# Kernel optimization log

Measured on AMD Instinct MI355X. Metric: run time of the kernel, lower is better.

The kernel has to match this reference:

```python
import math
import jax, jax.numpy as jnp
import numpy as np

N_HEAD = 32
LAYER_NUMBER = 10  # cancels out: beta*alibi*L + alpha*QK^T*L = alibi + QK^T/sqrt(d)


def build_alibi(seq_len, n_head, dtype):
    # Faithful port of BLOOM's build_alibi_tensor -> [n_head, 1, seq_len]
    cp2 = 2 ** math.floor(math.log2(n_head))
    base = 2.0 ** (-(2.0 ** -(math.log2(cp2) - 3)))
    slopes = base ** np.arange(1, 1 + cp2)
    if cp2 != n_head:
        extra_base = 2.0 ** (-(2.0 ** -(math.log2(2 * cp2) - 3)))
        num_rem = min(cp2, n_head - cp2)
        slopes = np.concatenate([slopes, extra_base ** np.arange(1, 1 + 2 * num_rem, 2)])
    alibi = slopes[:, None, None] * np.arange(seq_len)[None, None, :]
    return jnp.asarray(alibi, dtype)


def setup_inputs() -> dict:
    key = jax.random.key(0)
    ks = jax.random.split(key, 6)
    B, S, H = 4, 1024, 4096
    return {
        "hidden_states": jax.random.normal(ks[0], (B, S, H), jnp.float32),
        "residual": jax.random.normal(ks[1], (B, S, H), jnp.float32),
        "qkv_w": jax.random.normal(ks[2], (3 * H, H), jnp.float32) * 0.02,
        "qkv_b": jnp.zeros((3 * H,), jnp.float32),
        "dense_w": jax.random.normal(ks[3], (H, H), jnp.float32) * 0.02,
        "dense_b": jnp.zeros((H,), jnp.float32),
    }


def reference(hidden_states, residual, qkv_w, qkv_b, dense_w, dense_b):
    B, S, H = hidden_states.shape
    nh = N_HEAD
    d = H // nh
    # fused qkv projection: [B,S,3H] -> [B,S,nh,3d] -> split
    mixed = (hidden_states @ qkv_w.T + qkv_b).reshape(B, S, nh, 3 * d)
    q, k, v = jnp.split(mixed, 3, axis=-1)  # each [B,S,nh,d]

    alibi = build_alibi(S, nh, hidden_states.dtype)  # [nh,1,S]
    # beta*alibi + alpha*QK^T, then *layer_number in scaled softmax == alibi + QK^T/sqrt(d)
    scores = jnp.einsum("bqhd,bkhd->bhqk", q, k) / math.sqrt(d) + alibi[None]  # [B,nh,S,S]

    causal = jnp.tril(jnp.ones((S, S), bool))  # [S,S], True = attend
    scores = jnp.where(causal, scores, jnp.asarray(-10000.0, scores.dtype))
    # softmax in fp32 (attention_softmax_in_fp32), then zero masked entries like *(~padded_causal_mask)
    probs = jax.nn.softmax(scores.astype(jnp.float32), axis=-1) * causal
    probs = probs.astype(v.dtype)

    ctx = jnp.einsum("bhqk,bkhd->bqhd", probs, v).reshape(B, S, H)
    out = ctx @ dense_w.T + dense_b + residual  # dropout_add with p=0 / eval
    return out
```

## Files before the change

### kernel.cpp

```cpp
#include <hip/hip_runtime.h>
#include <hip/hip_bf16.h>

typedef __attribute__((ext_vector_type(8))) short bf16x8;
typedef __attribute__((ext_vector_type(4))) short short4v;
typedef __attribute__((ext_vector_type(4))) float f32x4;

#define MFMA16(A, B, C) __builtin_amdgcn_mfma_f32_16x16x32_bf16((A), (B), (C), 0, 0, 0)
#define GLDS16(g, l)                                                            \
  __builtin_amdgcn_global_load_lds(                                             \
      (const __attribute__((address_space(1))) void*)(g),                       \
      (__attribute__((address_space(3))) void*)(l), 16, 0, 0)

__device__ __forceinline__ short f2bf(float f) {
  union { float f; unsigned u; } v; v.f = f;
  return (short)((v.u + 0x7fffu + ((v.u >> 16) & 1u)) >> 16);
}

__device__ __forceinline__ void blk_barrier() {
  asm volatile("" ::: "memory");
  __builtin_amdgcn_s_barrier();
  asm volatile("" ::: "memory");
}

__global__ __launch_bounds__(256) void cvt_kernel(const float* __restrict__ in,
                                                  short* __restrict__ out, int n4) {
  int i = blockIdx.x * 256 + threadIdx.x;
  const int stride = gridDim.x * 256;
  for (; i < n4; i += stride) {
    f32x4 v = ((const f32x4*)in)[i];
    short4v o;
    o[0] = f2bf(v[0]); o[1] = f2bf(v[1]); o[2] = f2bf(v[2]); o[3] = f2bf(v[3]);
    ((short4v*)out)[i] = o;
  }
}

__global__ __launch_bounds__(512, 2) void gemm_bt8(const short* __restrict__ A,
                                                   const short* __restrict__ B,
                                                   const float* __restrict__ bias,
                                                   const float* __restrict__ resid,
                                                   short* __restrict__ Cb,
                                                   float* __restrict__ Cf,
                                                   int Mtiles, int Nn, int K, int mode) {
  __shared__ short sA[2][2][8192];
  __shared__ short sB[2][2][8192];
  const int tid = threadIdx.x;
  const int w = tid >> 6, l = tid & 63;
  const int wm = w >> 2, wn = w & 3;
  const int fr = l & 15, g4 = l >> 4, sx = l & 7;

  const int nwg = gridDim.x;
  const int qq = nwg >> 3, rr = nwg & 7;
  const int xcd = blockIdx.x & 7, sub = blockIdx.x >> 3;
  const int swz = (xcd < rr ? xcd * (qq + 1) : rr * (qq + 1) + (xcd - rr) * qq) + sub;
  const int rowBase = (swz % Mtiles) * 256;
  const int colBase = (swz / Mtiles) * 256;

  const int NT = K >> 6;
  const int swcol = ((l & 7) ^ (l >> 3)) * 8;
  const short* Ag = A + (size_t)(rowBase + w * 8 + (l >> 3)) * K + swcol;
  const short* Bg = B + (size_t)(colBase + w * 8 + (l >> 3)) * K + swcol;
  const size_t q1 = (size_t)64 * K;
  const size_t hh = (size_t)128 * K;

#define STAGE_A(buf, h, ko)                                     \
  GLDS16(Ag + (h) * hh + (ko), &sA[buf][h][w * 512]);           \
  GLDS16(Ag + (h) * hh + q1 + (ko), &sA[buf][h][(8 + w) * 512]);
#define STAGE_B(buf, h, ko)                                     \
  GLDS16(Bg + (h) * hh + (ko), &sB[buf][h][w * 512]);           \
  GLDS16(Bg + (h) * hh + q1 + (ko), &sB[buf][h][(8 + w) * 512]);
#define RD_A(buf, m, ks) \
  (*(const bf16x8*)&sA[buf][wm][(((m) * 16 + fr) << 6) + ((((ks) * 4 + g4) ^ sx) << 3)])
#define RD_B(buf, nf, ks) \
  (*(const bf16x8*)&sB[buf][wn >> 1][((((wn & 1) * 64) + (nf) * 16 + fr) << 6) + ((((ks) * 4 + g4) ^ sx) << 3)])

  f32x4 acc[8][4];
#pragma unroll
  for (int m = 0; m < 8; m++)
#pragma unroll
    for (int n = 0; n < 4; n++) acc[m][n] = (f32x4)(0.0f);

  STAGE_A(0, 0, 0); STAGE_A(0, 1, 0);
  STAGE_B(0, 0, 0); STAGE_B(0, 1, 0);

  for (int t = 0; t < NT; ++t) {
    const int cur = t & 1, nxt = cur ^ 1;
    const size_t ko = (size_t)(t + 1) << 6;
    bf16x8 bfr[4][2], af[2][2];
    if (t + 1 < NT) {
      STAGE_A(nxt, 0, ko); STAGE_A(nxt, 1, ko);
      asm volatile("s_waitcnt vmcnt(4)" ::: "memory");
    } else {
      asm volatile("s_waitcnt vmcnt(0)" ::: "memory");
    }
    blk_barrier();
#pragma unroll
    for (int nf = 0; nf < 4; nf++) {
      bfr[nf][0] = RD_B(cur, nf, 0);
      bfr[nf][1] = RD_B(cur, nf, 1);
    }
    af[0][0] = RD_A(cur, 0, 0); af[0][1] = RD_A(cur, 0, 1);
    af[1][0] = RD_A(cur, 1, 0); af[1][1] = RD_A(cur, 1, 1);
    __builtin_amdgcn_s_setprio(1);
#pragma unroll
    for (int mi = 0; mi < 2; mi++)
#pragma unroll
      for (int nf = 0; nf < 4; nf++) {
        acc[mi][nf] = MFMA16(af[mi][0], bfr[nf][0], acc[mi][nf]);
        acc[mi][nf] = MFMA16(af[mi][1], bfr[nf][1], acc[mi][nf]);
      }
    __builtin_amdgcn_s_setprio(0);
    blk_barrier();
#pragma unroll
    for (int p = 1; p < 4; p++) {
      af[0][0] = RD_A(cur, 2 * p, 0);     af[0][1] = RD_A(cur, 2 * p, 1);
      af[1][0] = RD_A(cur, 2 * p + 1, 0); af[1][1] = RD_A(cur, 2 * p + 1, 1);
      if (p == 1 && t + 1 < NT) {
        STAGE_B(nxt, 0, ko); STAGE_B(nxt, 1, ko);
      }
      blk_barrier();
      __builtin_amdgcn_s_setprio(1);
#pragma unroll
      for (int mi = 0; mi < 2; mi++)
#pragma unroll
        for (int nf = 0; nf < 4; nf++) {
          acc[2 * p + mi][nf] = MFMA16(af[mi][0], bfr[nf][0], acc[2 * p + mi][nf]);
          acc[2 * p + mi][nf] = MFMA16(af[mi][1], bfr[nf][1], acc[2 * p + mi][nf]);
        }
      __builtin_amdgcn_s_setprio(0);
      blk_barrier();
    }
  }

#pragma unroll
  for (int m = 0; m < 8; m++) {
    const int row0 = rowBase + wm * 128 + m * 16 + g4 * 4;
#pragma unroll
    for (int n = 0; n < 4; n++) {
      const int col = colBase + wn * 64 + n * 16 + fr;
      const float bc = bias[col];
#pragma unroll
      for (int j = 0; j < 4; j++) {
        const size_t idx = (size_t)(row0 + j) * Nn + col;
        const float v = acc[m][n][j] + bc;
        if (mode == 0) Cb[idx] = f2bf(v);
        else Cf[idx] = v + resid[idx];
      }
    }
  }
#undef STAGE_A
#undef STAGE_B
#undef RD_A
#undef RD_B
}

__global__ __launch_bounds__(512, 4) void gemm_bt(const short* __restrict__ A,
                                                  const short* __restrict__ B,
                                                  const float* __restrict__ bias,
                                                  const float* __restrict__ resid,
                                                  short* __restrict__ Cb,
                                                  float* __restrict__ Cf,
                                                  int Mtiles, int Nn, int K, int mode) {
  __shared__ short sA[2][128 * 32];
  __shared__ short sB[2][256 * 32];
  const int tid = threadIdx.x;
  const int w = tid >> 6, l = tid & 63;
  const int wm = w >> 2, wn = w & 3;
  const int fr = l & 15, g4 = l >> 4;
  const int slotx = (g4 ^ ((fr >> 1) & 3)) << 3;

  const int nwg = gridDim.x;
  const int qq = nwg >> 3, rr = nwg & 7;
  const int xcd = blockIdx.x & 7, sub = blockIdx.x >> 3;
  const int swz = (xcd < rr ? xcd * (qq + 1) : rr * (qq + 1) + (xcd - rr) * qq) + sub;
  const int rowBase = (swz % Mtiles) * 128;
  const int colBase = (swz / Mtiles) * 256;

  const int NT = K >> 5;
  const int scol = ((l & 3) ^ ((l >> 3) & 3)) << 3;
  const short* Ag = A + (size_t)(rowBase + w * 16 + (l >> 2)) * K + scol;
  const short* Bg0 = B + (size_t)(colBase + w * 16 + (l >> 2)) * K + scol;
  const short* Bg1 = Bg0 + (size_t)128 * K;

  f32x4 acc[4][4];
#pragma unroll
  for (int m = 0; m < 4; m++)
#pragma unroll
    for (int n = 0; n < 4; n++) acc[m][n] = (f32x4)(0.0f);

  GLDS16(Ag, &sA[0][w * 512]);
  GLDS16(Bg0, &sB[0][w * 512]);
  GLDS16(Bg1, &sB[0][(8 + w) * 512]);

  for (int t = 0; t < NT; ++t) {
    const int cur = t & 1, nxt = cur ^ 1;
    const int ko = (t + 1) << 5;
    if (t + 1 < NT) {
      GLDS16(Ag + ko, &sA[nxt][w * 512]);
      GLDS16(Bg0 + ko, &sB[nxt][w * 512]);
      GLDS16(Bg1 + ko, &sB[nxt][(8 + w) * 512]);
      asm volatile("s_waitcnt vmcnt(3)" ::: "memory");
    } else {
      asm volatile("s_waitcnt vmcnt(0)" ::: "memory");
    }
    blk_barrier();

    bf16x8 af[4], bfr[4];
#pragma unroll
    for (int m = 0; m < 4; m++)
      af[m] = *(const bf16x8*)&sA[cur][(wm * 64 + m * 16 + fr) * 32 + slotx];
#pragma unroll
    for (int nf = 0; nf < 4; nf++)
      bfr[nf] = *(const bf16x8*)&sB[cur][(wn * 64 + nf * 16 + fr) * 32 + slotx];
    __builtin_amdgcn_s_setprio(1);
#pragma unroll
    for (int m = 0; m < 4; m++)
#pragma unroll
      for (int nf = 0; nf < 4; nf++)
        acc[m][nf] = MFMA16(af[m], bfr[nf], acc[m][nf]);
    __builtin_amdgcn_s_setprio(0);
    blk_barrier();
  }

#pragma unroll
  for (int m = 0; m < 4; m++) {
    const int row0 = rowBase + wm * 64 + m * 16 + g4 * 4;
#pragma unroll
    for (int n = 0; n < 4; n++) {
      const int col = colBase + wn * 64 + n * 16 + fr;
      const float bc = bias[col];
#pragma unroll
      for (int j = 0; j < 4; j++) {
        const size_t idx = (size_t)(row0 + j) * Nn + col;
        const float v = acc[m][n][j] + bc;
        if (mode == 0) Cb[idx] = f2bf(v);
        else Cf[idx] = v + resid[idx];
      }
    }
  }
}

__global__ __launch_bounds__(256) void vtrans_kernel(const short* __restrict__ mixed,
                                                     short* __restrict__ vt) {
  __shared__ short tl[64][132];
  const int tid = threadIdx.x;
  const int st = blockIdx.x;
  const int bh = blockIdx.y;
  const int b = bh >> 5, h = bh & 31;
  const short* src = mixed + (size_t)(b * 1024 + st * 64) * 12288 + h * 384 + 256;
#pragma unroll
  for (int it = 0; it < 8; it++) {
    int idx = (tid + it * 256) * 4;
    int row = idx >> 7, col = idx & 127;
    *(short4v*)&tl[row][col] = *(const short4v*)(src + row * 12288 + col);
  }
  __syncthreads();
  short* dst = vt + (size_t)bh * 128 * 1024 + st * 64;
#pragma unroll
  for (int it = 0; it < 8; it++) {
    int o = (tid + it * 256) * 4;
    int d = o >> 6, t4 = o & 63;
    short4v w;
    w[0] = tl[t4][d]; w[1] = tl[t4 + 1][d]; w[2] = tl[t4 + 2][d]; w[3] = tl[t4 + 3][d];
    *(short4v*)(dst + d * 1024 + t4) = w;
  }
}

__global__ __launch_bounds__(256, 2) void attn_kernel(const short* __restrict__ mixed,
                                                      const short* __restrict__ vt,
                                                      short* __restrict__ ctx) {
  __shared__ short sK[2][64 * 128];
  __shared__ short sV[2][128 * 64];
  __shared__ unsigned p_lds[4][16 * 36];
  const int tid = threadIdx.x;
  const int w = tid >> 6, l = tid & 63;
  const int g = l >> 4, f = l & 15, f7 = l & 7;

  const int bidx = blockIdx.x;
  const int xcd = bidx & 7, idx = bidx >> 3;
  const int bh = (xcd << 4) | (idx >> 4);
  const int qt = idx & 15;
  const int b = bh >> 5, h = bh & 31;
  const int qw = qt * 64 + w * 16;
  const float scale = 0.08838834764831845f;
  const float slope = exp2f(-0.25f * (float)(h + 1));

  const short* qptr = mixed + (size_t)b * 1024 * 12288 + h * 384;
  const short* kptr = qptr + 128;
  const short* vtp = vt + (size_t)bh * 128 * 1024;

  bf16x8 qf[4];
  {
    const short* qrow = qptr + (size_t)(qw + f) * 12288 + (g << 3);
#pragma unroll
    for (int ks = 0; ks < 4; ks++) qf[ks] = *(const bf16x8*)(qrow + ks * 32);
  }

#define STAGE_K(buf, kt)                                                        \
  {                                                                             \
    _Pragma("unroll") for (int c4 = 0; c4 < 4; c4++) {                          \
      const int c = c4 * 4 + w;                                                 \
      const int r = c * 4 + (l >> 4);                                           \
      GLDS16(kptr + (size_t)((kt) + r) * 12288 + (((l & 15) ^ (r & 7)) << 3),   \
             &sK[buf][c << 9]);                                                 \
    }                                                                           \
  }
#define STAGE_V(buf, kt)                                                        \
  {                                                                             \
    _Pragma("unroll") for (int c4 = 0; c4 < 4; c4++) {                          \
      const int c = c4 * 4 + w;                                                 \
      const int r = c * 8 + (l >> 3);                                           \
      GLDS16(vtp + (size_t)r * 1024 + (kt) + (((l & 7) ^ (r & 7)) << 3),        \
             &sV[buf][c << 9]);                                                 \
    }                                                                           \
  }

  f32x4 acc[8];
#pragma unroll
  for (int n = 0; n < 8; n++) acc[n] = (f32x4)(0.0f);
  float mrun = -1e30f, lrun = 0.0f;
  const int q = qw + f;
  unsigned* pw = p_lds[w];

  const int TT = qt + 1;
  STAGE_K(0, 0);
  STAGE_V(0, 0);

  for (int t = 0; t < TT; ++t) {
    const int cur = t & 1, nxt = cur ^ 1;
    const int kt = t << 6;
    if (t + 1 < TT) {
      STAGE_K(nxt, kt + 64);
      STAGE_V(nxt, kt + 64);
      asm volatile("s_waitcnt vmcnt(8)" ::: "memory");
    } else {
      asm volatile("s_waitcnt vmcnt(0)" ::: "memory");
    }
    blk_barrier();

    f32x4 s[4];
#pragma unroll
    for (int ksub = 0; ksub < 4; ksub++) {
      s[ksub] = (f32x4)(0.0f);
      const int r = ksub * 16 + f;
#pragma unroll
      for (int ks = 0; ks < 4; ks++) {
        bf16x8 kf = *(const bf16x8*)&sK[cur][(r << 7) + ((((ks << 2) + g) ^ f7) << 3)];
        s[ksub] = MFMA16(kf, qf[ks], s[ksub]);
      }
    }

    float ev[4][4];
    float tmax = -1e30f;
#pragma unroll
    for (int ksub = 0; ksub < 4; ksub++)
#pragma unroll
      for (int j = 0; j < 4; j++) {
        const int k = kt + ksub * 16 + g * 4 + j;
        float v = s[ksub][j] * scale + slope * (float)k;
        if (k > q) v = -1e30f;
        ev[ksub][j] = v;
        tmax = fmaxf(tmax, v);
      }
    tmax = fmaxf(tmax, __shfl_xor(tmax, 16));
    tmax = fmaxf(tmax, __shfl_xor(tmax, 32));
    const float mnew = fmaxf(mrun, tmax);
    const float asc = __expf(mrun - mnew);
    float psum = 0.0f;
    unsigned* pr = pw + f * 36;
#pragma unroll
    for (int ksub = 0; ksub < 4; ksub++) {
      float e0 = __expf(ev[ksub][0] - mnew);
      float e1 = __expf(ev[ksub][1] - mnew);
      float e2 = __expf(ev[ksub][2] - mnew);
      float e3 = __expf(ev[ksub][3] - mnew);
      psum += (e0 + e1) + (e2 + e3);
      unsigned w0 = (unsigned)(unsigned short)f2bf(e0) |
                    ((unsigned)(unsigned short)f2bf(e1) << 16);
      unsigned w1 = (unsigned)(unsigned short)f2bf(e2) |
                    ((unsigned)(unsigned short)f2bf(e3) << 16);
      pr[ksub * 8 + g * 2] = w0;
      pr[ksub * 8 + g * 2 + 1] = w1;
    }
    psum += __shfl_xor(psum, 16);
    psum += __shfl_xor(psum, 32);
    lrun = lrun * asc + psum;
    mrun = mnew;

    float ascB[4];
#pragma unroll
    for (int j = 0; j < 4; j++) ascB[j] = __shfl(asc, 20 * g + j);
#pragma unroll
    for (int n = 0; n < 8; n++)
#pragma unroll
      for (int j = 0; j < 4; j++) acc[n][j] *= ascB[j];

    bf16x8 pa0 = *(const bf16x8*)(pw + f * 36 + (g << 2));
    bf16x8 pa1 = *(const bf16x8*)(pw + f * 36 + 16 + (g << 2));
#pragma unroll
    for (int n = 0; n < 8; n++) {
      const int dr = (n << 4) + f;
      bf16x8 vf0 = *(const bf16x8*)&sV[cur][(dr << 6) + ((g ^ f7) << 3)];
      acc[n] = MFMA16(pa0, vf0, acc[n]);
      bf16x8 vf1 = *(const bf16x8*)&sV[cur][(dr << 6) + (((4 + g) ^ f7) << 3)];
      acc[n] = MFMA16(pa1, vf1, acc[n]);
    }
    blk_barrier();
  }

  const float linv = 1.0f / lrun;
  float invB[4];
#pragma unroll
  for (int j = 0; j < 4; j++) invB[j] = __shfl(linv, 20 * g + j);
  const int trow = b * 1024 + qw + (g << 2);
#pragma unroll
  for (int n = 0; n < 8; n++) {
    const int col = h * 128 + (n << 4) + f;
#pragma unroll
    for (int j = 0; j < 4; j++)
      ctx[(size_t)(trow + j) * 4096 + col] = f2bf(acc[n][j] * invB[j]);
  }
#undef STAGE_K
#undef STAGE_V
}

extern "C" void kernel_launch(void* const* d_in, const int* in_sizes, int n_in,
                              void* d_out, int out_size, void* d_ws, size_t ws_size,
                              hipStream_t stream) {
  const float* hs = (const float*)d_in[0];
  const float* resid = (const float*)d_in[1];
  const float* qkv_w = (const float*)d_in[2];
  const float* qkv_b = (const float*)d_in[3];
  const float* dense_w = (const float*)d_in[4];
  const float* dense_b = (const float*)d_in[5];
  float* out = (float*)d_out;

  short* hs_b = (short*)d_ws;
  short* wqkv_b = hs_b + (size_t)16777216;
  short* wd_b = wqkv_b + (size_t)50331648;
  short* mixed = wd_b + (size_t)16777216;
  short* vt = wqkv_b;
  short* ctx = hs_b;

  cvt_kernel<<<1024, 256, 0, stream>>>(hs, hs_b, 16777216 / 4);
  cvt_kernel<<<1024, 256, 0, stream>>>(qkv_w, wqkv_b, 50331648 / 4);
  cvt_kernel<<<1024, 256, 0, stream>>>(dense_w, wd_b, 16777216 / 4);
  gemm_bt8<<<dim3(48 * 16), 512, 0, stream>>>(hs_b, wqkv_b, qkv_b, nullptr,
                                              mixed, nullptr, 16, 12288, 4096, 0);
  vtrans_kernel<<<dim3(16, 128), 256, 0, stream>>>(mixed, vt);
  attn_kernel<<<2048, 256, 0, stream>>>(mixed, vt, ctx);
  gemm_bt<<<dim3(32 * 16), 512, 0, stream>>>(ctx, wd_b, dense_b, resid,
                                             nullptr, out, 32, 4096, 4096, 1);
}
```

Before: 791.1 us.

## Software-pipeline LDS fragment reads ahead of MFMA in GEMM main loop

Restructures the GEMM K-loop so that LDS fragment reads for the next MFMA group are issued right after the current group's MFMAs, and the first fragments of the next K tile are preloaded at the end of each iteration. The per-iteration vmcnt wait moves to the end of the loop, just before the next tile's fragments are read. The aim is to hide LDS read latency behind MFMA execution and to cut some barrier stalls. Fewer barriers now separate the reads of one buffer from the async global-to-LDS writes into the other, so correctness depends on careful ordering of those barriers.

```diff
diff --git a/kernel.cpp b/kernel.cpp
--- a/kernel.cpp
+++ b/kernel.cpp
@@ -81,25 +81,24 @@
 
   STAGE_A(0, 0, 0); STAGE_A(0, 1, 0);
   STAGE_B(0, 0, 0); STAGE_B(0, 1, 0);
+  asm volatile("s_waitcnt vmcnt(0)" ::: "memory");
+  blk_barrier();
+
+  bf16x8 bfr[4][2], af[2][2];
+#pragma unroll
+  for (int nf = 0; nf < 4; nf++) {
+    bfr[nf][0] = RD_B(0, nf, 0);
+    bfr[nf][1] = RD_B(0, nf, 1);
+  }
+  af[0][0] = RD_A(0, 0, 0); af[0][1] = RD_A(0, 0, 1);
+  af[1][0] = RD_A(0, 1, 0); af[1][1] = RD_A(0, 1, 1);
 
   for (int t = 0; t < NT; ++t) {
     const int cur = t & 1, nxt = cur ^ 1;
     const size_t ko = (size_t)(t + 1) << 6;
-    bf16x8 bfr[4][2], af[2][2];
-    if (t + 1 < NT) {
-      STAGE_A(nxt, 0, ko); STAGE_A(nxt, 1, ko);
-      asm volatile("s_waitcnt vmcnt(4)" ::: "memory");
-    } else {
-      asm volatile("s_waitcnt vmcnt(0)" ::: "memory");
-    }
-    blk_barrier();
-#pragma unroll
-    for (int nf = 0; nf < 4; nf++) {
-      bfr[nf][0] = RD_B(cur, nf, 0);
-      bfr[nf][1] = RD_B(cur, nf, 1);
-    }
-    af[0][0] = RD_A(cur, 0, 0); af[0][1] = RD_A(cur, 0, 1);
-    af[1][0] = RD_A(cur, 1, 0); af[1][1] = RD_A(cur, 1, 1);
+    const bool more = (t + 1 < NT);
+
+    if (more) { STAGE_A(nxt, 0, ko); STAGE_A(nxt, 1, ko); }
     __builtin_amdgcn_s_setprio(1);
 #pragma unroll
     for (int mi = 0; mi < 2; mi++)
@@ -109,26 +108,58 @@
         acc[mi][nf] = MFMA16(af[mi][1], bfr[nf][1], acc[mi][nf]);
       }
     __builtin_amdgcn_s_setprio(0);
-    blk_barrier();
-#pragma unroll
-    for (int p = 1; p < 4; p++) {
-      af[0][0] = RD_A(cur, 2 * p, 0);     af[0][1] = RD_A(cur, 2 * p, 1);
-      af[1][0] = RD_A(cur, 2 * p + 1, 0); af[1][1] = RD_A(cur, 2 * p + 1, 1);
-      if (p == 1 && t + 1 < NT) {
-        STAGE_B(nxt, 0, ko); STAGE_B(nxt, 1, ko);
-      }
-      blk_barrier();
-      __builtin_amdgcn_s_setprio(1);
-#pragma unroll
-      for (int mi = 0; mi < 2; mi++)
-#pragma unroll
-        for (int nf = 0; nf < 4; nf++) {
-          acc[2 * p + mi][nf] = MFMA16(af[mi][0], bfr[nf][0], acc[2 * p + mi][nf]);
-          acc[2 * p + mi][nf] = MFMA16(af[mi][1], bfr[nf][1], acc[2 * p + mi][nf]);
-        }
-      __builtin_amdgcn_s_setprio(0);
-      blk_barrier();
-    }
+    af[0][0] = RD_A(cur, 2, 0); af[0][1] = RD_A(cur, 2, 1);
+    af[1][0] = RD_A(cur, 3, 0); af[1][1] = RD_A(cur, 3, 1);
+    blk_barrier();
+
+    if (more) { STAGE_B(nxt, 0, ko); STAGE_B(nxt, 1, ko); }
+    __builtin_amdgcn_s_setprio(1);
+#pragma unroll
+    for (int mi = 0; mi < 2; mi++)
+#pragma unroll
+      for (int nf = 0; nf < 4; nf++) {
+        acc[2 + mi][nf] = MFMA16(af[mi][0], bfr[nf][0], acc[2 + mi][nf]);
+        acc[2 + mi][nf] = MFMA16(af[mi][1], bfr[nf][1], acc[2 + mi][nf]);
+      }
+    __builtin_amdgcn_s_setprio(0);
+    af[0][0] = RD_A(cur, 4, 0); af[0][1] = RD_A(cur, 4, 1);
+    af[1][0] = RD_A(cur, 5, 0); af[1][1] = RD_A(cur, 5, 1);
+    blk_barrier();
+
+    __builtin_amdgcn_s_setprio(1);
+#pragma unroll
+    for (int mi = 0; mi < 2; mi++)
+#pragma unroll
+      for (int nf = 0; nf < 4; nf++) {
+        acc[4 + mi][nf] = MFMA16(af[mi][0], bfr[nf][0], acc[4 + mi][nf]);
+        acc[4 + mi][nf] = MFMA16(af[mi][1], bfr[nf][1], acc[4 + mi][nf]);
+      }
+    __builtin_amdgcn_s_setprio(0);
+    af[0][0] = RD_A(cur, 6, 0); af[0][1] = RD_A(cur, 6, 1);
+    af[1][0] = RD_A(cur, 7, 0); af[1][1] = RD_A(cur, 7, 1);
+    blk_barrier();
+
+    if (more) asm volatile("s_waitcnt vmcnt(0)" ::: "memory");
+    blk_barrier();
+    __builtin_amdgcn_s_setprio(1);
+#pragma unroll
+    for (int mi = 0; mi < 2; mi++)
+#pragma unroll
+      for (int nf = 0; nf < 4; nf++) {
+        acc[6 + mi][nf] = MFMA16(af[mi][0], bfr[nf][0], acc[6 + mi][nf]);
+        acc[6 + mi][nf] = MFMA16(af[mi][1], bfr[nf][1], acc[6 + mi][nf]);
+      }
+    __builtin_amdgcn_s_setprio(0);
+    if (more) {
+#pragma unroll
+      for (int nf = 0; nf < 4; nf++) {
+        bfr[nf][0] = RD_B(nxt, nf, 0);
+        bfr[nf][1] = RD_B(nxt, nf, 1);
+      }
+      af[0][0] = RD_A(nxt, 0, 0); af[0][1] = RD_A(nxt, 0, 1);
+      af[1][0] = RD_A(nxt, 1, 0); af[1][1] = RD_A(nxt, 1, 1);
+    }
+    blk_barrier();
   }
 
 #pragma unroll
```

Measured after the change: 861.4 us. +8.9%, slower.

## Process two 16-row query subtiles per wave in attention to reuse K/V tiles

Applied to the files above, without the earlier changes.

Each attention block now covers 128 query rows instead of 64: each wave holds two 16-row Q fragments with separate online-softmax state and accumulators, and the grid is halved to 1024 blocks. Every K/V tile staged into LDS is consumed twice, which halves global K/V traffic and barrier count per query row. The cost is more registers (two accumulator sets), lower occupancy, fewer blocks for load balancing, and extra fully masked work on the causal diagonal tile for the first subtile.

```diff
diff --git a/kernel.cpp b/kernel.cpp
--- a/kernel.cpp
+++ b/kernel.cpp
@@ -277,10 +277,10 @@
 
   const int bidx = blockIdx.x;
   const int xcd = bidx & 7, idx = bidx >> 3;
-  const int bh = (xcd << 4) | (idx >> 4);
-  const int qt = idx & 15;
+  const int bh = (xcd << 4) | (idx >> 3);
+  const int qt = idx & 7;
   const int b = bh >> 5, h = bh & 31;
-  const int qw = qt * 64 + w * 16;
+  const int qwave = qt * 128 + w * 32;
   const float scale = 0.08838834764831845f;
   const float slope = exp2f(-0.25f * (float)(h + 1));
 
@@ -288,11 +288,12 @@
   const short* kptr = qptr + 128;
   const short* vtp = vt + (size_t)bh * 128 * 1024;
 
-  bf16x8 qf[4];
-  {
-    const short* qrow = qptr + (size_t)(qw + f) * 12288 + (g << 3);
-#pragma unroll
-    for (int ks = 0; ks < 4; ks++) qf[ks] = *(const bf16x8*)(qrow + ks * 32);
+  bf16x8 qf[2][4];
+#pragma unroll
+  for (int e = 0; e < 2; e++) {
+    const short* qrow = qptr + (size_t)(qwave + 16 * e + f) * 12288 + (g << 3);
+#pragma unroll
+    for (int ks = 0; ks < 4; ks++) qf[e][ks] = *(const bf16x8*)(qrow + ks * 32);
   }
 
 #define STAGE_K(buf, kt)                                                        \
@@ -314,14 +315,15 @@
     }                                                                           \
   }
 
-  f32x4 acc[8];
-#pragma unroll
-  for (int n = 0; n < 8; n++) acc[n] = (f32x4)(0.0f);
-  float mrun = -1e30f, lrun = 0.0f;
-  const int q = qw + f;
+  f32x4 acc[2][8];
+#pragma unroll
+  for (int e = 0; e < 2; e++)
+#pragma unroll
+    for (int n = 0; n < 8; n++) acc[e][n] = (f32x4)(0.0f);
+  float mrun[2] = {-1e30f, -1e30f}, lrun[2] = {0.0f, 0.0f};
   unsigned* pw = p_lds[w];
 
-  const int TT = qt + 1;
+  const int TT = 2 * qt + 2;
   STAGE_K(0, 0);
   STAGE_V(0, 0);
 
@@ -337,87 +339,99 @@
     }
     blk_barrier();
 
-    f32x4 s[4];
-#pragma unroll
-    for (int ksub = 0; ksub < 4; ksub++) {
-      s[ksub] = (f32x4)(0.0f);
-      const int r = ksub * 16 + f;
-#pragma unroll
-      for (int ks = 0; ks < 4; ks++) {
-        bf16x8 kf = *(const bf16x8*)&sK[cur][(r << 7) + ((((ks << 2) + g) ^ f7) << 3)];
-        s[ksub] = MFMA16(kf, qf[ks], s[ksub]);
-      }
-    }
-
-    float ev[4][4];
-    float tmax = -1e30f;
-#pragma unroll
-    for (int ksub = 0; ksub < 4; ksub++)
-#pragma unroll
-      for (int j = 0; j < 4; j++) {
-        const int k = kt + ksub * 16 + g * 4 + j;
-        float v = s[ksub][j] * scale + slope * (float)k;
-        if (k > q) v = -1e30f;
-        ev[ksub][j] = v;
-        tmax = fmaxf(tmax, v);
-      }
-    tmax = fmaxf(tmax, __shfl_xor(tmax, 16));
-    tmax = fmaxf(tmax, __shfl_xor(tmax, 32));
-    const float mnew = fmaxf(mrun, tmax);
-    const float asc = __expf(mrun - mnew);
-    float psum = 0.0f;
-    unsigned* pr = pw + f * 36;
-#pragma unroll
-    for (int ksub = 0; ksub < 4; ksub++) {
-      float e0 = __expf(ev[ksub][0] - mnew);
-      float e1 = __expf(ev[ksub][1] - mnew);
-      float e2 = __expf(ev[ksub][2] - mnew);
-      float e3 = __expf(ev[ksub][3] - mnew);
-      psum += (e0 + e1) + (e2 + e3);
-      unsigned w0 = (unsigned)(unsigned short)f2bf(e0) |
-                    ((unsigned)(unsigned short)f2bf(e1) << 16);
-      unsigned w1 = (unsigned)(unsigned short)f2bf(e2) |
-                    ((unsigned)(unsigned short)f2bf(e3) << 16);
-      pr[ksub * 8 + g * 2] = w0;
-      pr[ksub * 8 + g * 2 + 1] = w1;
-    }
-    psum += __shfl_xor(psum, 16);
-    psum += __shfl_xor(psum, 32);
-    lrun = lrun * asc + psum;
-    mrun = mnew;
-
-    float ascB[4];
-#pragma unroll
-    for (int j = 0; j < 4; j++) ascB[j] = __shfl(asc, 20 * g + j);
-#pragma unroll
-    for (int n = 0; n < 8; n++)
-#pragma unroll
-      for (int j = 0; j < 4; j++) acc[n][j] *= ascB[j];
-
-    bf16x8 pa0 = *(const bf16x8*)(pw + f * 36 + (g << 2));
-    bf16x8 pa1 = *(const bf16x8*)(pw + f * 36 + 16 + (g << 2));
+#pragma unroll
+    for (int e = 0; e < 2; e++) {
+      asm volatile("" ::: "memory");
+
+      const int q = qwave + 16 * e + f;
+
+      f32x4 s[4];
+#pragma unroll
+      for (int ksub = 0; ksub < 4; ksub++) {
+        s[ksub] = (f32x4)(0.0f);
+        const int r = ksub * 16 + f;
+#pragma unroll
+        for (int ks = 0; ks < 4; ks++) {
+          bf16x8 kf = *(const bf16x8*)&sK[cur][(r << 7) + ((((ks << 2) + g) ^ f7) << 3)];
+          s[ksub] = MFMA16(kf, qf[e][ks], s[ksub]);
+        }
+      }
+
+      float ev[4][4];
+      float tmax = -1e30f;
+#pragma unroll
+      for (int ksub = 0; ksub < 4; ksub++)
+#pragma unroll
+        for (int j = 0; j < 4; j++) {
+          const int k = kt + ksub * 16 + g * 4 + j;
+          float v = s[ksub][j] * scale + slope * (float)k;
+          if (k > q) v = -1e30f;
+          ev[ksub][j] = v;
+          tmax = fmaxf(tmax, v);
+        }
+      tmax = fmaxf(tmax, __shfl_xor(tmax, 16));
+      tmax = fmaxf(tmax, __shfl_xor(tmax, 32));
+      const float mnew = fmaxf(mrun[e], tmax);
+      const float asc = __expf(mrun[e] - mnew);
+      float psum = 0.0f;
+      unsigned* pr = pw + f * 36;
+#pragma unroll
+      for (int ksub = 0; ksub < 4; ksub++) {
+        float e0 = __expf(ev[ksub][0] - mnew);
+        float e1 = __expf(ev[ksub][1] - mnew);
+        float e2 = __expf(ev[ksub][2] - mnew);
+        float e3 = __expf(ev[ksub][3] - mnew);
+        psum += (e0 + e1) + (e2 + e3);
+        unsigned w0 = (unsigned)(unsigned short)f2bf(e0) |
+                      ((unsigned)(unsigned short)f2bf(e1) << 16);
+        unsigned w1 = (unsigned)(unsigned short)f2bf(e2) |
+                      ((unsigned)(unsigned short)f2bf(e3) << 16);
+        pr[ksub * 8 + g * 2] = w0;
+        pr[ksub * 8 + g * 2 + 1] = w1;
+      }
+      psum += __shfl_xor(psum, 16);
+      psum += __shfl_xor(psum, 32);
+      lrun[e] = lrun[e] * asc + psum;
+      mrun[e] = mnew;
+
+      float ascB[4];
+#pragma unroll
+      for (int j = 0; j < 4; j++) ascB[j] = __shfl(asc, 20 * g + j);
+#pragma unroll
+      for (int n = 0; n < 8; n++)
+#pragma unroll
+        for (int j = 0; j < 4; j++) acc[e][n][j] *= ascB[j];
+
+      asm volatile("" ::: "memory");
+
+      bf16x8 pa0 = *(const bf16x8*)(pw + f * 36 + (g << 2));
+      bf16x8 pa1 = *(const bf16x8*)(pw + f * 36 + 16 + (g << 2));
+#pragma unroll
+      for (int n = 0; n < 8; n++) {
+        const int dr = (n << 4) + f;
+        bf16x8 vf0 = *(const bf16x8*)&sV[cur][(dr << 6) + ((g ^ f7) << 3)];
+        acc[e][n] = MFMA16(pa0, vf0, acc[e][n]);
+        bf16x8 vf1 = *(const bf16x8*)&sV[cur][(dr << 6) + (((4 + g) ^ f7) << 3)];
+        acc[e][n] = MFMA16(pa1, vf1, acc[e][n]);
+      }
+    }
+    blk_barrier();
+  }
+
+#pragma unroll
+  for (int e = 0; e < 2; e++) {
+    const float linv = 1.0f / lrun[e];
+    float invB[4];
+#pragma unroll
+    for (int j = 0; j < 4; j++) invB[j] = __shfl(linv, 20 * g + j);
+    const int trow = b * 1024 + qwave + 16 * e + (g << 2);
 #pragma unroll
     for (int n = 0; n < 8; n++) {
-      const int dr = (n << 4) + f;
-      bf16x8 vf0 = *(const bf16x8*)&sV[cur][(dr << 6) + ((g ^ f7) << 3)];
-      acc[n] = MFMA16(pa0, vf0, acc[n]);
-      bf16x8 vf1 = *(const bf16x8*)&sV[cur][(dr << 6) + (((4 + g) ^ f7) << 3)];
-      acc[n] = MFMA16(pa1, vf1, acc[n]);
-    }
-    blk_barrier();
-  }
-
-  const float linv = 1.0f / lrun;
-  float invB[4];
-#pragma unroll
-  for (int j = 0; j < 4; j++) invB[j] = __shfl(linv, 20 * g + j);
-  const int trow = b * 1024 + qw + (g << 2);
-#pragma unroll
-  for (int n = 0; n < 8; n++) {
-    const int col = h * 128 + (n << 4) + f;
-#pragma unroll
-    for (int j = 0; j < 4; j++)
-      ctx[(size_t)(trow + j) * 4096 + col] = f2bf(acc[n][j] * invB[j]);
+      const int col = h * 128 + (n << 4) + f;
+#pragma unroll
+      for (int j = 0; j < 4; j++)
+        ctx[(size_t)(trow + j) * 4096 + col] = f2bf(acc[e][n][j] * invB[j]);
+    }
   }
 #undef STAGE_K
 #undef STAGE_V
@@ -447,7 +461,7 @@
   gemm_bt8<<<dim3(48 * 16), 512, 0, stream>>>(hs_b, wqkv_b, qkv_b, nullptr,
                                               mixed, nullptr, 16, 12288, 4096, 0);
   vtrans_kernel<<<dim3(16, 128), 256, 0, stream>>>(mixed, vt);
-  attn_kernel<<<2048, 256, 0, stream>>>(mixed, vt, ctx);
+  attn_kernel<<<1024, 256, 0, stream>>>(mixed, vt, ctx);
   gemm_bt<<<dim3(32 * 16), 512, 0, stream>>>(ctx, wd_b, dense_b, resid,
                                              nullptr, out, 32, 4096, 4096, 1);
 }
```

New measurement: 802.0 us. About the same (+1.4%).
